# Kernel optimization log

Hardware: AMD Instinct MI355X
Metric: run time of the kernel (lower is better)

## Reference

```python
import jax, jax.numpy as jnp
import numpy as np

N_NODES = 100000
N_EDGES = 6400000
TOKEN_DIM = 16


def setup_inputs() -> dict:
    key = jax.random.key(0)
    k1, k2, k3, k4, k5 = jax.random.split(key, 5)
    x = jax.random.normal(k1, (N_NODES, 1), dtype=jnp.float32)
    edge_index = jax.random.randint(k2, (2, N_EDGES), 0, N_NODES, dtype=jnp.int64)
    # PyTorch nn.Linear init: U(-1/sqrt(fan_in), 1/sqrt(fan_in)); plain normals are fine for a correctness baseline
    w1 = jax.random.normal(k3, (TOKEN_DIM, 2), dtype=jnp.float32) * (1.0 / np.sqrt(2.0))
    b1 = jnp.zeros((TOKEN_DIM,), dtype=jnp.float32)
    w2 = jax.random.normal(k4, (TOKEN_DIM, TOKEN_DIM), dtype=jnp.float32) * (1.0 / np.sqrt(TOKEN_DIM))
    b2 = jnp.zeros((TOKEN_DIM,), dtype=jnp.float32)
    return {"x": x, "edge_index": edge_index, "w1": w1, "b1": b1, "w2": w2, "b2": b2}


def reference(x, edge_index, w1, b1, w2, b2):
    row, col = edge_index[0], edge_index[1]
    # gather-multiply: bond_e = s_row * s_col, shape [E, 1]
    bond = x[row] * x[col]
    # scatter-add into local_field, shape [N, 1]
    local_field = jax.ops.segment_sum(bond, row, num_segments=x.shape[0])
    feats = jnp.concatenate([x, local_field], axis=1)  # [N, 2]
    h = jax.nn.relu(feats @ w1.T + b1)                  # [N, token_dim]
    tokens = jax.nn.relu(h @ w2.T + b2)                 # [N, token_dim]
    return tokens
```

## Files before the change

kernel.cpp:

```cpp
#include <hip/hip_runtime.h>
#include <hip/hip_bf16.h>

#define TOKEN_DIM 16
#define RANGES 5
#define MAX_RS 20000
#define MAX_C  102

__global__ __launch_bounds__(1024, 8)
void nit_phase1(const int* __restrict__ row, const int* __restrict__ col,
                const float* __restrict__ x,
                unsigned short* __restrict__ partial,
                int N, long long E, int chunkE, int RS) {
    __shared__ float acc[MAX_RS];
    const int c = blockIdx.x / RANGES;
    const int r = blockIdx.x % RANGES;
    const int base = r * RS;
    int cnt = N - base; if (cnt > RS) cnt = RS; if (cnt < 0) cnt = 0;
    const int t = threadIdx.x, nt = blockDim.x;

    for (int j = t; j < cnt; j += nt) acc[j] = 0.0f;
    __syncthreads();

    long long i0 = (long long)c * chunkE;
    long long i1 = i0 + chunkE; if (i1 > E) i1 = E;
    long long len = (i1 > i0) ? (i1 - i0) : 0;
    long long ngrp = len >> 3;

    long long g = t;
    int4 r0a, r1a, c0a, c1a;
    if (g < ngrp) {
        long long idx = i0 + (g << 3);
        r0a = *reinterpret_cast<const int4*>(row + idx);
        r1a = *reinterpret_cast<const int4*>(row + idx + 4);
        c0a = *reinterpret_cast<const int4*>(col + idx);
        c1a = *reinterpret_cast<const int4*>(col + idx + 4);
    }
    while (g < ngrp) {
        const long long gn = g + nt;
        int4 r0b, r1b, c0b, c1b;
        if (gn < ngrp) {
            long long idx = i0 + (gn << 3);
            r0b = *reinterpret_cast<const int4*>(row + idx);
            r1b = *reinterpret_cast<const int4*>(row + idx + 4);
            c0b = *reinterpret_cast<const int4*>(col + idx);
            c1b = *reinterpret_cast<const int4*>(col + idx + 4);
        }
        unsigned d;
        d = (unsigned)(r0a.x - base); if (d < (unsigned)cnt) atomicAdd(&acc[d], x[c0a.x]);
        d = (unsigned)(r0a.y - base); if (d < (unsigned)cnt) atomicAdd(&acc[d], x[c0a.y]);
        d = (unsigned)(r0a.z - base); if (d < (unsigned)cnt) atomicAdd(&acc[d], x[c0a.z]);
        d = (unsigned)(r0a.w - base); if (d < (unsigned)cnt) atomicAdd(&acc[d], x[c0a.w]);
        d = (unsigned)(r1a.x - base); if (d < (unsigned)cnt) atomicAdd(&acc[d], x[c1a.x]);
        d = (unsigned)(r1a.y - base); if (d < (unsigned)cnt) atomicAdd(&acc[d], x[c1a.y]);
        d = (unsigned)(r1a.z - base); if (d < (unsigned)cnt) atomicAdd(&acc[d], x[c1a.z]);
        d = (unsigned)(r1a.w - base); if (d < (unsigned)cnt) atomicAdd(&acc[d], x[c1a.w]);
        r0a = r0b; r1a = r1b; c0a = c0b; c1a = c1b;
        g = gn;
    }
    for (long long idx = i0 + (ngrp << 3) + t; idx < i1; idx += nt) {
        unsigned d = (unsigned)(row[idx] - base);
        if (d < (unsigned)cnt) atomicAdd(&acc[d], x[col[idx]]);
    }
    __syncthreads();

    unsigned short* dst = partial + (size_t)c * N + base;
    for (int j = t; j < cnt; j += nt) {
        __hip_bfloat16 h = __float2bfloat16(acc[j]);
        __builtin_nontemporal_store(*reinterpret_cast<unsigned short*>(&h), dst + j);
    }
}

__global__ __launch_bounds__(256, 8)
void nit_phase2(const float* __restrict__ x,
                const unsigned short* __restrict__ partial,
                const float* __restrict__ w1, const float* __restrict__ b1,
                const float* __restrict__ w2, const float* __restrict__ b2,
                float* __restrict__ out, int N, int C) {
    __shared__ float sw1[TOKEN_DIM * 2];
    __shared__ float sb1[TOKEN_DIM];
    __shared__ float sw2[TOKEN_DIM * TOKEN_DIM];
    __shared__ float sb2[TOKEN_DIM];
    __shared__ float red[256];

    const int t = threadIdx.x;
    if (t < TOKEN_DIM * TOKEN_DIM) sw2[t] = w2[t];
    if (t < TOKEN_DIM * 2) sw1[t] = w1[t];
    if (t < TOKEN_DIM) { sb1[t] = b1[t]; sb2[t] = b2[t]; }

    const int n = t & 63;
    const int g = t >> 6;
    const int node0 = blockIdx.x * 64;
    const int node = node0 + n;

    float s = 0.0f;
    if (node < N) {
#pragma unroll 4
        for (int c = g; c < C; c += 4) {
            unsigned short u = __builtin_nontemporal_load(partial + (size_t)c * N + node);
            s += __uint_as_float(((unsigned)u) << 16);
        }
    }
    red[t] = s;
    __syncthreads();

    if (t < 64) {
        const int nn = node0 + t;
        if (nn < N) {
            const float ssum = red[t] + red[64 + t] + red[128 + t] + red[192 + t];
            const float xv = x[nn];
            const float lv = xv * ssum;

            float h[TOKEN_DIM];
#pragma unroll
            for (int j = 0; j < TOKEN_DIM; ++j) {
                float v = fmaf(xv, sw1[2 * j], fmaf(lv, sw1[2 * j + 1], sb1[j]));
                h[j] = v > 0.0f ? v : 0.0f;
            }

            float o[TOKEN_DIM];
#pragma unroll
            for (int j = 0; j < TOKEN_DIM; ++j) {
                float v = sb2[j];
#pragma unroll
                for (int k = 0; k < TOKEN_DIM; ++k)
                    v = fmaf(h[k], sw2[j * TOKEN_DIM + k], v);
                o[j] = v > 0.0f ? v : 0.0f;
            }

            float4* op = reinterpret_cast<float4*>(out + (size_t)nn * TOKEN_DIM);
#pragma unroll
            for (int j = 0; j < 4; ++j)
                op[j] = make_float4(o[4 * j], o[4 * j + 1], o[4 * j + 2], o[4 * j + 3]);
        }
    }
}

extern "C" void kernel_launch(void* const* d_in, const int* in_sizes, int n_in,
                              void* d_out, int out_size, void* d_ws, size_t ws_size,
                              hipStream_t stream) {
    const float* x  = (const float*)d_in[0];
    const int*   ei = (const int*)d_in[1];
    const float* w1 = (const float*)d_in[2];
    const float* b1 = (const float*)d_in[3];
    const float* w2 = (const float*)d_in[4];
    const float* b2 = (const float*)d_in[5];
    float* out = (float*)d_out;

    const int N = in_sizes[0];
    const long long E = in_sizes[1] / 2;
    const int* row = ei;
    const int* col = ei + E;

    long long maxC = (long long)(ws_size / ((size_t)N * sizeof(unsigned short)));
    int C = maxC < 1 ? 1 : (maxC > MAX_C ? MAX_C : (int)maxC);
    const int RS = (N + RANGES - 1) / RANGES;
    long long ce = (E + C - 1) / C;
    int chunkE = (int)((ce + 7LL) & ~7LL);

    unsigned short* partial = (unsigned short*)d_ws;

    nit_phase1<<<C * RANGES, 1024, 0, stream>>>(row, col, x, partial,
                                                N, E, chunkE, RS);

    int grid2 = (N + 63) / 64;
    nit_phase2<<<grid2, 256, 0, stream>>>(x, partial, w1, b1, w2, b2,
                                          out, N, C);
}
```

Before: 158.7 us.

## Map edge chunks to XCDs for L2 reuse and make phase-1 atomics branchless

```diff
diff --git a/kernel.cpp b/kernel.cpp
--- a/kernel.cpp
+++ b/kernel.cpp
@@ -4,69 +4,99 @@
 #define TOKEN_DIM 16
 #define RANGES 5
 #define MAX_RS 20000
-#define MAX_C  102
+#define DUMMY  32
+#define MAX_C  96
+#define NXCD   8
 
 __global__ __launch_bounds__(1024, 8)
 void nit_phase1(const int* __restrict__ row, const int* __restrict__ col,
                 const float* __restrict__ x,
                 unsigned short* __restrict__ partial,
-                int N, long long E, int chunkE, int RS) {
-    __shared__ float acc[MAX_RS];
-    const int c = blockIdx.x / RANGES;
-    const int r = blockIdx.x % RANGES;
+                int N, long long E, int chunkE, int RS, int C) {
+    __shared__ float acc[MAX_RS + DUMMY];
+    const int b = blockIdx.x;
+    const int k = b % NXCD;
+    const int s = b / NXCD;
+    const int r = s % RANGES;
+    const int c = k + NXCD * (s / RANGES);
+    if (c >= C) return;
+
     const int base = r * RS;
     int cnt = N - base; if (cnt > RS) cnt = RS; if (cnt < 0) cnt = 0;
     const int t = threadIdx.x, nt = blockDim.x;
 
     for (int j = t; j < cnt; j += nt) acc[j] = 0.0f;
+    if (t < DUMMY) acc[RS + t] = 0.0f;
     __syncthreads();
 
     long long i0 = (long long)c * chunkE;
     long long i1 = i0 + chunkE; if (i1 > E) i1 = E;
     long long len = (i1 > i0) ? (i1 - i0) : 0;
     long long ngrp = len >> 3;
-
-    long long g = t;
-    int4 r0a, r1a, c0a, c1a;
-    if (g < ngrp) {
-        long long idx = i0 + (g << 3);
-        r0a = *reinterpret_cast<const int4*>(row + idx);
-        r1a = *reinterpret_cast<const int4*>(row + idx + 4);
-        c0a = *reinterpret_cast<const int4*>(col + idx);
-        c1a = *reinterpret_cast<const int4*>(col + idx + 4);
-    }
-    while (g < ngrp) {
-        const long long gn = g + nt;
-        int4 r0b, r1b, c0b, c1b;
-        if (gn < ngrp) {
-            long long idx = i0 + (gn << 3);
-            r0b = *reinterpret_cast<const int4*>(row + idx);
-            r1b = *reinterpret_cast<const int4*>(row + idx + 4);
-            c0b = *reinterpret_cast<const int4*>(col + idx);
-            c1b = *reinterpret_cast<const int4*>(col + idx + 4);
-        }
-        unsigned d;
-        d = (unsigned)(r0a.x - base); if (d < (unsigned)cnt) atomicAdd(&acc[d], x[c0a.x]);
-        d = (unsigned)(r0a.y - base); if (d < (unsigned)cnt) atomicAdd(&acc[d], x[c0a.y]);
-        d = (unsigned)(r0a.z - base); if (d < (unsigned)cnt) atomicAdd(&acc[d], x[c0a.z]);
-        d = (unsigned)(r0a.w - base); if (d < (unsigned)cnt) atomicAdd(&acc[d], x[c0a.w]);
-        d = (unsigned)(r1a.x - base); if (d < (unsigned)cnt) atomicAdd(&acc[d], x[c1a.x]);
-        d = (unsigned)(r1a.y - base); if (d < (unsigned)cnt) atomicAdd(&acc[d], x[c1a.y]);
-        d = (unsigned)(r1a.z - base); if (d < (unsigned)cnt) atomicAdd(&acc[d], x[c1a.z]);
-        d = (unsigned)(r1a.w - base); if (d < (unsigned)cnt) atomicAdd(&acc[d], x[c1a.w]);
-        r0a = r0b; r1a = r1b; c0a = c0b; c1a = c1b;
-        g = gn;
+    const unsigned ucnt = (unsigned)cnt;
+    const int dummy = RS + (t & (DUMMY - 1));
+
+    for (long long g = t; g < ngrp; g += nt) {
+        const long long idx = i0 + (g << 3);
+        const int4 r0 = *reinterpret_cast<const int4*>(row + idx);
+        const int4 r1 = *reinterpret_cast<const int4*>(row + idx + 4);
+        const int4 c0 = *reinterpret_cast<const int4*>(col + idx);
+        const int4 c1 = *reinterpret_cast<const int4*>(col + idx + 4);
+
+        const unsigned d0 = (unsigned)(r0.x - base);
+        const unsigned d1 = (unsigned)(r0.y - base);
+        const unsigned d2 = (unsigned)(r0.z - base);
+        const unsigned d3 = (unsigned)(r0.w - base);
+        const unsigned d4 = (unsigned)(r1.x - base);
+        const unsigned d5 = (unsigned)(r1.y - base);
+        const unsigned d6 = (unsigned)(r1.z - base);
+        const unsigned d7 = (unsigned)(r1.w - base);
+
+        const float v0 = x[d0 < ucnt ? c0.x : 0];
+        const float v1 = x[d1 < ucnt ? c0.y : 0];
+        const float v2 = x[d2 < ucnt ? c0.z : 0];
+        const float v3 = x[d3 < ucnt ? c0.w : 0];
+        const float v4 = x[d4 < ucnt ? c1.x : 0];
+        const float v5 = x[d5 < ucnt ? c1.y : 0];
+        const float v6 = x[d6 < ucnt ? c1.z : 0];
+        const float v7 = x[d7 < ucnt ? c1.w : 0];
+
+        atomicAdd(&acc[d0 < ucnt ? (int)d0 : dummy], d0 < ucnt ? v0 : 0.0f);
+        atomicAdd(&acc[d1 < ucnt ? (int)d1 : dummy], d1 < ucnt ? v1 : 0.0f);
+        atomicAdd(&acc[d2 < ucnt ? (int)d2 : dummy], d2 < ucnt ? v2 : 0.0f);
+        atomicAdd(&acc[d3 < ucnt ? (int)d3 : dummy], d3 < ucnt ? v3 : 0.0f);
+        atomicAdd(&acc[d4 < ucnt ? (int)d4 : dummy], d4 < ucnt ? v4 : 0.0f);
+        atomicAdd(&acc[d5 < ucnt ? (int)d5 : dummy], d5 < ucnt ? v5 : 0.0f);
+        atomicAdd(&acc[d6 < ucnt ? (int)d6 : dummy], d6 < ucnt ? v6 : 0.0f);
+        atomicAdd(&acc[d7 < ucnt ? (int)d7 : dummy], d7 < ucnt ? v7 : 0.0f);
     }
     for (long long idx = i0 + (ngrp << 3) + t; idx < i1; idx += nt) {
         unsigned d = (unsigned)(row[idx] - base);
-        if (d < (unsigned)cnt) atomicAdd(&acc[d], x[col[idx]]);
+        if (d < ucnt) atomicAdd(&acc[d], x[col[idx]]);
     }
     __syncthreads();
 
     unsigned short* dst = partial + (size_t)c * N + base;
-    for (int j = t; j < cnt; j += nt) {
-        __hip_bfloat16 h = __float2bfloat16(acc[j]);
-        __builtin_nontemporal_store(*reinterpret_cast<unsigned short*>(&h), dst + j);
+    const bool vec_ok = ((((size_t)c * N + base) & 1) == 0);
+    if (vec_ok) {
+        const int cnt2 = cnt >> 1;
+        unsigned int* dst2 = reinterpret_cast<unsigned int*>(dst);
+        for (int j = t; j < cnt2; j += nt) {
+            __hip_bfloat16 ha = __float2bfloat16(acc[2 * j]);
+            __hip_bfloat16 hb = __float2bfloat16(acc[2 * j + 1]);
+            unsigned int w = (unsigned int)(*reinterpret_cast<unsigned short*>(&ha))
+                           | ((unsigned int)(*reinterpret_cast<unsigned short*>(&hb)) << 16);
+            __builtin_nontemporal_store(w, dst2 + j);
+        }
+        if ((cnt & 1) && t == 0) {
+            __hip_bfloat16 h = __float2bfloat16(acc[cnt - 1]);
+            __builtin_nontemporal_store(*reinterpret_cast<unsigned short*>(&h), dst + cnt - 1);
+        }
+    } else {
+        for (int j = t; j < cnt; j += nt) {
+            __hip_bfloat16 h = __float2bfloat16(acc[j]);
+            __builtin_nontemporal_store(*reinterpret_cast<unsigned short*>(&h), dst + j);
+        }
     }
 }
 
@@ -153,14 +183,16 @@
 
     long long maxC = (long long)(ws_size / ((size_t)N * sizeof(unsigned short)));
     int C = maxC < 1 ? 1 : (maxC > MAX_C ? MAX_C : (int)maxC);
-    const int RS = (N + RANGES - 1) / RANGES;
+    int RS = ((N + RANGES - 1) / RANGES + 1) & ~1;
     long long ce = (E + C - 1) / C;
     int chunkE = (int)((ce + 7LL) & ~7LL);
 
     unsigned short* partial = (unsigned short*)d_ws;
 
-    nit_phase1<<<C * RANGES, 1024, 0, stream>>>(row, col, x, partial,
-                                                N, E, chunkE, RS);
+    const int cg = (C + NXCD - 1) / NXCD;
+    const int grid1 = NXCD * RANGES * cg;
+    nit_phase1<<<grid1, 1024, 0, stream>>>(row, col, x, partial,
+                                           N, E, chunkE, RS, C);
 
     int grid2 = (N + 63) / 64;
     nit_phase2<<<grid2, 256, 0, stream>>>(x, partial, w1, b1, w2, b2,
```

Result: slower. 281.1 us (+77.1%).

## Replace LDS range-partitioned accumulation with global atomics into replicated partial arrays

Applied to the files above, without the earlier changes.

```diff
diff --git a/kernel.cpp b/kernel.cpp
--- a/kernel.cpp
+++ b/kernel.cpp
@@ -1,137 +1,98 @@
 #include <hip/hip_runtime.h>
-#include <hip/hip_bf16.h>
 
 #define TOKEN_DIM 16
-#define RANGES 5
-#define MAX_RS 20000
-#define MAX_C  102
+#define NPART 8
 
-__global__ __launch_bounds__(1024, 8)
+typedef float floatx4 __attribute__((ext_vector_type(4)));
+
+__global__ __launch_bounds__(256, 8)
 void nit_phase1(const int* __restrict__ row, const int* __restrict__ col,
-                const float* __restrict__ x,
-                unsigned short* __restrict__ partial,
-                int N, long long E, int chunkE, int RS) {
-    __shared__ float acc[MAX_RS];
-    const int c = blockIdx.x / RANGES;
-    const int r = blockIdx.x % RANGES;
-    const int base = r * RS;
-    int cnt = N - base; if (cnt > RS) cnt = RS; if (cnt < 0) cnt = 0;
-    const int t = threadIdx.x, nt = blockDim.x;
+                const float* __restrict__ x, float* __restrict__ partial,
+                int N, long long E) {
+    const long long gtid = (long long)blockIdx.x * blockDim.x + threadIdx.x;
+    const long long gstride = (long long)gridDim.x * blockDim.x;
+    float* __restrict__ mypart = partial + (size_t)(blockIdx.x & (NPART - 1)) * N;
 
-    for (int j = t; j < cnt; j += nt) acc[j] = 0.0f;
-    __syncthreads();
+    const long long ngrp = E >> 3;
+    for (long long g = gtid; g < ngrp; g += gstride) {
+        const long long idx = g << 3;
+        const int4 r0 = *reinterpret_cast<const int4*>(row + idx);
+        const int4 r1 = *reinterpret_cast<const int4*>(row + idx + 4);
+        const int4 c0 = *reinterpret_cast<const int4*>(col + idx);
+        const int4 c1 = *reinterpret_cast<const int4*>(col + idx + 4);
 
-    long long i0 = (long long)c * chunkE;
-    long long i1 = i0 + chunkE; if (i1 > E) i1 = E;
-    long long len = (i1 > i0) ? (i1 - i0) : 0;
-    long long ngrp = len >> 3;
+        const float v0 = x[c0.x];
+        const float v1 = x[c0.y];
+        const float v2 = x[c0.z];
+        const float v3 = x[c0.w];
+        const float v4 = x[c1.x];
+        const float v5 = x[c1.y];
+        const float v6 = x[c1.z];
+        const float v7 = x[c1.w];
 
-    long long g = t;
-    int4 r0a, r1a, c0a, c1a;
-    if (g < ngrp) {
-        long long idx = i0 + (g << 3);
-        r0a = *reinterpret_cast<const int4*>(row + idx);
-        r1a = *reinterpret_cast<const int4*>(row + idx + 4);
-        c0a = *reinterpret_cast<const int4*>(col + idx);
-        c1a = *reinterpret_cast<const int4*>(col + idx + 4);
+        atomicAdd(mypart + r0.x, v0);
+        atomicAdd(mypart + r0.y, v1);
+        atomicAdd(mypart + r0.z, v2);
+        atomicAdd(mypart + r0.w, v3);
+        atomicAdd(mypart + r1.x, v4);
+        atomicAdd(mypart + r1.y, v5);
+        atomicAdd(mypart + r1.z, v6);
+        atomicAdd(mypart + r1.w, v7);
     }
-    while (g < ngrp) {
-        const long long gn = g + nt;
-        int4 r0b, r1b, c0b, c1b;
-        if (gn < ngrp) {
-            long long idx = i0 + (gn << 3);
-            r0b = *reinterpret_cast<const int4*>(row + idx);
-            r1b = *reinterpret_cast<const int4*>(row + idx + 4);
-            c0b = *reinterpret_cast<const int4*>(col + idx);
-            c1b = *reinterpret_cast<const int4*>(col + idx + 4);
-        }
-        unsigned d;
-        d = (unsigned)(r0a.x - base); if (d < (unsigned)cnt) atomicAdd(&acc[d], x[c0a.x]);
-        d = (unsigned)(r0a.y - base); if (d < (unsigned)cnt) atomicAdd(&acc[d], x[c0a.y]);
-        d = (unsigned)(r0a.z - base); if (d < (unsigned)cnt) atomicAdd(&acc[d], x[c0a.z]);
-        d = (unsigned)(r0a.w - base); if (d < (unsigned)cnt) atomicAdd(&acc[d], x[c0a.w]);
-        d = (unsigned)(r1a.x - base); if (d < (unsigned)cnt) atomicAdd(&acc[d], x[c1a.x]);
-        d = (unsigned)(r1a.y - base); if (d < (unsigned)cnt) atomicAdd(&acc[d], x[c1a.y]);
-        d = (unsigned)(r1a.z - base); if (d < (unsigned)cnt) atomicAdd(&acc[d], x[c1a.z]);
-        d = (unsigned)(r1a.w - base); if (d < (unsigned)cnt) atomicAdd(&acc[d], x[c1a.w]);
-        r0a = r0b; r1a = r1b; c0a = c0b; c1a = c1b;
-        g = gn;
-    }
-    for (long long idx = i0 + (ngrp << 3) + t; idx < i1; idx += nt) {
-        unsigned d = (unsigned)(row[idx] - base);
-        if (d < (unsigned)cnt) atomicAdd(&acc[d], x[col[idx]]);
-    }
-    __syncthreads();
-
-    unsigned short* dst = partial + (size_t)c * N + base;
-    for (int j = t; j < cnt; j += nt) {
-        __hip_bfloat16 h = __float2bfloat16(acc[j]);
-        __builtin_nontemporal_store(*reinterpret_cast<unsigned short*>(&h), dst + j);
-    }
+    for (long long idx = (ngrp << 3) + gtid; idx < E; idx += gstride)
+        atomicAdd(mypart + row[idx], x[col[idx]]);
 }
 
 __global__ __launch_bounds__(256, 8)
 void nit_phase2(const float* __restrict__ x,
-                const unsigned short* __restrict__ partial,
+                const float* __restrict__ partial,
                 const float* __restrict__ w1, const float* __restrict__ b1,
                 const float* __restrict__ w2, const float* __restrict__ b2,
-                float* __restrict__ out, int N, int C) {
+                float* __restrict__ out, int N) {
     __shared__ float sw1[TOKEN_DIM * 2];
     __shared__ float sb1[TOKEN_DIM];
     __shared__ float sw2[TOKEN_DIM * TOKEN_DIM];
     __shared__ float sb2[TOKEN_DIM];
-    __shared__ float red[256];
 
     const int t = threadIdx.x;
     if (t < TOKEN_DIM * TOKEN_DIM) sw2[t] = w2[t];
     if (t < TOKEN_DIM * 2) sw1[t] = w1[t];
     if (t < TOKEN_DIM) { sb1[t] = b1[t]; sb2[t] = b2[t]; }
+    __syncthreads();
 
-    const int n = t & 63;
-    const int g = t >> 6;
-    const int node0 = blockIdx.x * 64;
-    const int node = node0 + n;
+    const int n = blockIdx.x * blockDim.x + t;
+    if (n >= N) return;
 
     float s = 0.0f;
-    if (node < N) {
-#pragma unroll 4
-        for (int c = g; c < C; c += 4) {
-            unsigned short u = __builtin_nontemporal_load(partial + (size_t)c * N + node);
-            s += __uint_as_float(((unsigned)u) << 16);
-        }
+#pragma unroll
+    for (int k = 0; k < NPART; ++k)
+        s += __builtin_nontemporal_load(partial + (size_t)k * N + n);
+
+    const float xv = x[n];
+    const float lv = xv * s;
+
+    float h[TOKEN_DIM];
+#pragma unroll
+    for (int j = 0; j < TOKEN_DIM; ++j) {
+        float v = fmaf(xv, sw1[2 * j], fmaf(lv, sw1[2 * j + 1], sb1[j]));
+        h[j] = v > 0.0f ? v : 0.0f;
     }
-    red[t] = s;
-    __syncthreads();
 
-    if (t < 64) {
-        const int nn = node0 + t;
-        if (nn < N) {
-            const float ssum = red[t] + red[64 + t] + red[128 + t] + red[192 + t];
-            const float xv = x[nn];
-            const float lv = xv * ssum;
+    float o[TOKEN_DIM];
+#pragma unroll
+    for (int j = 0; j < TOKEN_DIM; ++j) {
+        float v = sb2[j];
+#pragma unroll
+        for (int k = 0; k < TOKEN_DIM; ++k)
+            v = fmaf(h[k], sw2[j * TOKEN_DIM + k], v);
+        o[j] = v > 0.0f ? v : 0.0f;
+    }
 
-            float h[TOKEN_DIM];
+    floatx4* op = reinterpret_cast<floatx4*>(out + (size_t)n * TOKEN_DIM);
 #pragma unroll
-            for (int j = 0; j < TOKEN_DIM; ++j) {
-                float v = fmaf(xv, sw1[2 * j], fmaf(lv, sw1[2 * j + 1], sb1[j]));
-                h[j] = v > 0.0f ? v : 0.0f;
-            }
-
-            float o[TOKEN_DIM];
-#pragma unroll
-            for (int j = 0; j < TOKEN_DIM; ++j) {
-                float v = sb2[j];
-#pragma unroll
-                for (int k = 0; k < TOKEN_DIM; ++k)
-                    v = fmaf(h[k], sw2[j * TOKEN_DIM + k], v);
-                o[j] = v > 0.0f ? v : 0.0f;
-            }
-
-            float4* op = reinterpret_cast<float4*>(out + (size_t)nn * TOKEN_DIM);
-#pragma unroll
-            for (int j = 0; j < 4; ++j)
-                op[j] = make_float4(o[4 * j], o[4 * j + 1], o[4 * j + 2], o[4 * j + 3]);
-        }
+    for (int j = 0; j < 4; ++j) {
+        floatx4 w = { o[4 * j], o[4 * j + 1], o[4 * j + 2], o[4 * j + 3] };
+        __builtin_nontemporal_store(w, op + j);
     }
 }
 
@@ -151,18 +112,12 @@
     const int* row = ei;
     const int* col = ei + E;
 
-    long long maxC = (long long)(ws_size / ((size_t)N * sizeof(unsigned short)));
-    int C = maxC < 1 ? 1 : (maxC > MAX_C ? MAX_C : (int)maxC);
-    const int RS = (N + RANGES - 1) / RANGES;
-    long long ce = (E + C - 1) / C;
-    int chunkE = (int)((ce + 7LL) & ~7LL);
+    float* partial = (float*)d_ws;
 
-    unsigned short* partial = (unsigned short*)d_ws;
+    (void)hipMemsetAsync(partial, 0, (size_t)NPART * N * sizeof(float), stream);
 
-    nit_phase1<<<C * RANGES, 1024, 0, stream>>>(row, col, x, partial,
-                                                N, E, chunkE, RS);
+    nit_phase1<<<2048, 256, 0, stream>>>(row, col, x, partial, N, E);
 
-    int grid2 = (N + 63) / 64;
-    nit_phase2<<<grid2, 256, 0, stream>>>(x, partial, w1, b1, w2, b2,
-                                          out, N, C);
+    int grid2 = (N + 255) / 256;
+    nit_phase2<<<grid2, 256, 0, stream>>>(x, partial, w1, b1, w2, b2, out, N);
 }
```

Result: slower. 413.8 us (+160.7%).
